# Kernel tuning notes

Measured on AMD Instinct MI355X. Metric: run time of the kernel, lower is better.

Reference implementation:

```python
import jax, jax.numpy as jnp
import numpy as np

NUM_HEADS = 4
D_MODEL = 256
HEAD_DIM = D_MODEL // NUM_HEADS  # 64
B, N = 8, 2048


def _proj(x, W, b):
    # Conv1d with kernel_size=1 == pointwise linear over channel dim
    # x: [B, C_in, N], W: [C_out, C_in], b: [C_out]
    return jnp.einsum('oi,bin->bon', W, x) + b[None, :, None]


def setup_inputs() -> dict:
    key = jax.random.key(0)
    ks = jax.random.split(key, 11)
    s = 1.0 / np.sqrt(D_MODEL)
    return {
        'query': jax.random.normal(ks[0], (B, D_MODEL, N), jnp.float32),
        'key':   jax.random.normal(ks[1], (B, D_MODEL, N), jnp.float32),
        'value': jax.random.normal(ks[2], (B, D_MODEL, N), jnp.float32),
        'Wq': jax.random.normal(ks[3], (D_MODEL, D_MODEL), jnp.float32) * s,
        'bq': jax.random.normal(ks[4], (D_MODEL,), jnp.float32) * 0.01,
        'Wk': jax.random.normal(ks[5], (D_MODEL, D_MODEL), jnp.float32) * s,
        'bk': jax.random.normal(ks[6], (D_MODEL,), jnp.float32) * 0.01,
        'Wv': jax.random.normal(ks[7], (D_MODEL, D_MODEL), jnp.float32) * s,
        'bv': jax.random.normal(ks[8], (D_MODEL,), jnp.float32) * 0.01,
        'Wm': jax.random.normal(ks[9], (D_MODEL, D_MODEL), jnp.float32) * s,
        'bm': jax.random.normal(ks[10], (D_MODEL,), jnp.float32) * 0.01,
    }


def reference(query, key, value, Wq, bq, Wk, bk, Wv, bv, Wm, bm):
    b = query.shape[0]
    # project then split channels into (head_dim, num_heads): [B, d, h, N]
    q = _proj(query, Wq, bq).reshape(b, HEAD_DIM, NUM_HEADS, -1)
    k = _proj(key,   Wk, bk).reshape(b, HEAD_DIM, NUM_HEADS, -1)
    v = _proj(value, Wv, bv).reshape(b, HEAD_DIM, NUM_HEADS, -1)
    scale = 1.0 / jnp.sqrt(jnp.asarray(HEAD_DIM, q.dtype))
    scores = jnp.einsum('bdhn,bdhm->bhnm', q, k) * scale  # [B,H,N,N]
    prob = jax.nn.softmax(scores, axis=-1)
    x = jnp.einsum('bhnm,bdhm->bdhn', prob, v)  # [B,d,H,N]
    x = x.reshape(b, HEAD_DIM * NUM_HEADS, -1)  # [B, d_model, N]
    return _proj(x, Wm, bm)
```

## Files before the change

### kernel.cpp

```cpp
#include <hip/hip_runtime.h>
#include <math.h>


constexpr int BATCH  = 8;
constexpr int DMODEL = 256;
constexpr int SEQ    = 2048;
constexpr int HDIM   = 64;
constexpr int TN     = 128;
constexpr int TM     = 64;
constexpr int NJT    = SEQ / TM;

typedef _Float16 half4_t __attribute__((ext_vector_type(4)));
typedef _Float16 half8_t __attribute__((ext_vector_type(8)));
typedef float    float4_t __attribute__((ext_vector_type(4)));

static __device__ __forceinline__ void ld16_lds(const void* g, void* l) {
    __builtin_amdgcn_global_load_lds(
        (const __attribute__((address_space(1))) unsigned*)g,
        (__attribute__((address_space(3))) unsigned*)l, 16, 0, 0);
}

__global__ __launch_bounds__(256)
void prep_w(const float* __restrict__ Wq, const float* __restrict__ Wk,
            const float* __restrict__ Wv, const float* __restrict__ Wm,
            _Float16* __restrict__ wf)
{
    const int which = blockIdx.y;
    const float* src = which == 0 ? Wq : which == 1 ? Wk : which == 2 ? Wv : Wm;
    const int i = (blockIdx.x * 256 + threadIdx.x) * 4;
    const float4 v = *(const float4*)&src[i];
    half4_t o; o[0] = v.x; o[1] = v.y; o[2] = v.z; o[3] = v.w;
    *(half4_t*)&wf[(size_t)which * DMODEL * DMODEL + i] = o;
}

__global__ __launch_bounds__(256, 3)
void gemm_qkv(const _Float16* __restrict__ wf, const float* __restrict__ bq,
              const float* __restrict__ bk, const float* __restrict__ bv,
              const float* __restrict__ Xq, const float* __restrict__ Xk,
              const float* __restrict__ Xv, _Float16* __restrict__ qT,
              _Float16* __restrict__ kT, _Float16* __restrict__ vT)
{
    const int n0 = blockIdx.x * 64;
    const int proj = blockIdx.y >> 3, b = blockIdx.y & 7;
    const _Float16* W    = wf + (size_t)proj * DMODEL * DMODEL;
    const float*    bias = proj == 0 ? bq : proj == 1 ? bk : bv;
    const float*    X    = (proj == 0 ? Xq : proj == 1 ? Xk : Xv)
                           + (size_t)b * DMODEL * SEQ;
    const float qs = (proj == 0) ? 0.18033688011112042f : 1.0f;

    __shared__ __align__(16) char lds[50432];
    float*    T  = (float*)lds;
    _Float16* Xs = (_Float16*)(lds + 16640);
    _Float16* Tw = (_Float16*)lds;

    const int tid = threadIdx.x, tn = tid & 15, tc = tid >> 4;

    #pragma unroll
    for (int cc = 0; cc < 4; ++cc) {
        __syncthreads();
        #pragma unroll
        for (int i = 0; i < 4; ++i) {
            const int c = tc + 16 * i;
            const float4 v = *(const float4*)&X[(size_t)(cc * 64 + c) * SEQ + n0 + tn * 4];
            T[c * 65 + tn * 4 + 0] = v.x; T[c * 65 + tn * 4 + 1] = v.y;
            T[c * 65 + tn * 4 + 2] = v.z; T[c * 65 + tn * 4 + 3] = v.w;
        }
        __syncthreads();
        #pragma unroll
        for (int i = 0; i < 4; ++i) {
            const int n = tc + 16 * i;
            half4_t h4;
            #pragma unroll
            for (int j = 0; j < 4; ++j) h4[j] = (_Float16)T[(tn * 4 + j) * 65 + n];
            *(half4_t*)&Xs[n * 264 + cc * 64 + tn * 4] = h4;
        }
    }
    __syncthreads();

    const int w = tid >> 6, lane = tid & 63;
    const int lm = lane & 15, g = lane >> 4, g8 = g * 8;
    const int cw0 = w * 64;

    float4_t acc[4][4];
    #pragma unroll
    for (int mt = 0; mt < 4; ++mt)
        #pragma unroll
        for (int nt = 0; nt < 4; ++nt) acc[mt][nt] = (float4_t){0.f, 0.f, 0.f, 0.f};

    #pragma unroll
    for (int k0 = 0; k0 < DMODEL; k0 += 64) {
        half8_t a[4][2], bb[4][2];
        #pragma unroll
        for (int mt = 0; mt < 4; ++mt)
            #pragma unroll
            for (int kd = 0; kd < 2; ++kd)
                a[mt][kd] = *(const half8_t*)&W[(size_t)(cw0 + mt * 16 + lm) * DMODEL
                                                + k0 + kd * 32 + g8];
        #pragma unroll
        for (int nt = 0; nt < 4; ++nt)
            #pragma unroll
            for (int kd = 0; kd < 2; ++kd)
                bb[nt][kd] = *(const half8_t*)&Xs[(nt * 16 + lm) * 264
                                                  + k0 + kd * 32 + g8];
        #pragma unroll
        for (int kd = 0; kd < 2; ++kd)
            #pragma unroll
            for (int mt = 0; mt < 4; ++mt)
                #pragma unroll
                for (int nt = 0; nt < 4; ++nt)
                    acc[mt][nt] = __builtin_amdgcn_mfma_f32_16x16x32_f16(
                        a[mt][kd], bb[nt][kd], acc[mt][nt], 0, 0, 0);
    }
    __syncthreads();

    #pragma unroll
    for (int mt = 0; mt < 4; ++mt) {
        const float4 b4 = *(const float4*)&bias[cw0 + mt * 16 + g * 4];
        const float bb4[4] = {b4.x, b4.y, b4.z, b4.w};
        #pragma unroll
        for (int nt = 0; nt < 4; ++nt) {
            half4_t pk;
            #pragma unroll
            for (int r = 0; r < 4; ++r)
                pk[r] = (_Float16)((acc[mt][nt][r] + bb4[r]) * qs);
            *(half4_t*)&Tw[((w * 64 + nt * 16 + lm)) * 68 + mt * 16 + g * 4] = pk;
        }
    }

    if (proj < 2) {
        _Float16* dst = (proj == 0 ? qT : kT);
        const int h2 = lane >> 4, lml = lane & 15;
        #pragma unroll
        for (int it = 0; it < 4; ++it) {
            const int nl = it * 16 + lml;
            #pragma unroll
            for (int dc = 0; dc < 2; ++dc) {
                half8_t ch;
                #pragma unroll
                for (int e = 0; e < 8; ++e)
                    ch[e] = Tw[(w * 64 + nl) * 68 + 4 * (dc * 8 + e) + h2];
                const int chunk = (w * 2 + dc) ^ (nl & 7);
                *(half8_t*)&dst[((size_t)(b * 4 + h2) * SEQ + n0 + nl) * HDIM
                                + chunk * 8] = ch;
            }
        }
    } else {
        const int hh = lane & 3, dl = (lane >> 2) & 15;
        const int d = w * 16 + dl;
        const int hswap = ((dl >> 3) & 1) << 2;
        const size_t rowbase =
            (((size_t)(b * 4 + hh) * NJT + (n0 >> 6)) * HDIM + d) * (size_t)TM;
        #pragma unroll
        for (int jc = 0; jc < 8; ++jc) {
            half8_t ch;
            #pragma unroll
            for (int e = 0; e < 8; ++e)
                ch[e] = Tw[(w * 64 + jc * 8 + (e ^ hswap)) * 68 + 4 * dl + hh];
            *(half8_t*)&vT[rowbase + ((jc ^ (dl & 7)) << 3)] = ch;
        }
    }
}

__global__ __launch_bounds__(256, 4)
void attn_f16(const _Float16* __restrict__ qT, const _Float16* __restrict__ kT,
              const _Float16* __restrict__ vT, _Float16* __restrict__ xa,
              _Float16* __restrict__ xb, float* __restrict__ rs)
{
    const int lid = blockIdx.x;
    const int work = (lid & 7) * 128 + (lid >> 3);
    const int bh = work >> 5, b = bh >> 2, h = bh & 3;
    const int jh = (work >> 4) & 1;
    const int ib = work & 15;
    const int tid = threadIdx.x, wid = tid >> 6, lane = tid & 63;
    const int lm = lane & 15, g = lane >> 4;
    const int i0 = ib * TN + wid * 32;

    __shared__ _Float16 Kb[2][TM * HDIM];
    __shared__ _Float16 Vb[2][TM * HDIM];

    half8_t bq[2][2];
    const _Float16* qbase = qT + (size_t)bh * SEQ * HDIM;
    #pragma unroll
    for (int rt = 0; rt < 2; ++rt)
        #pragma unroll
        for (int kd = 0; kd < 2; ++kd) {
            const int row = i0 + rt * 16 + lm;
            bq[rt][kd] = *(const half8_t*)(qbase + (size_t)row * HDIM
                                           + (((kd * 4 + g) ^ (lm & 7)) << 3));
        }

    const char* kt = (const char*)(kT + ((size_t)bh * SEQ + jh * (SEQ / 2)) * HDIM);
    const char* vt = (const char*)(vT + ((size_t)bh * NJT + jh * 16) * TM * HDIM);

    float4_t o[2][4];
    float rsum[2] = {0.f, 0.f};
    #pragma unroll
    for (int rt = 0; rt < 2; ++rt)
        #pragma unroll
        for (int dt = 0; dt < 4; ++dt) o[rt][dt] = (float4_t){0.f, 0.f, 0.f, 0.f};

    #define STAGE(jt, bu)                                                     \
        {                                                                     \
            const char* kg = kt + (size_t)(jt) * 8192;                        \
            const char* vg = vt + (size_t)(jt) * 8192;                        \
            _Pragma("unroll")                                                 \
            for (int p = 0; p < 2; ++p) {                                     \
                const int c = wid + p * 4;                                    \
                ld16_lds(kg + c * 1024 + lane * 16, (char*)&Kb[bu][0] + c * 1024); \
                ld16_lds(vg + c * 1024 + lane * 16, (char*)&Vb[bu][0] + c * 1024); \
            }                                                                 \
        }

    STAGE(0, 0);
    __syncthreads();

    for (int jt = 0; jt < 16; ++jt) {
        const int cur = jt & 1;
        if (jt + 1 < 16) STAGE(jt + 1, cur ^ 1);

        float4_t s[4][2];
        #pragma unroll
        for (int ct = 0; ct < 4; ++ct)
            #pragma unroll
            for (int rt = 0; rt < 2; ++rt) s[ct][rt] = (float4_t){0.f, 0.f, 0.f, 0.f};
        #pragma unroll
        for (int kd = 0; kd < 2; ++kd)
            #pragma unroll
            for (int ct = 0; ct < 4; ++ct) {
                const half8_t fk = *(const half8_t*)
                    &Kb[cur][(ct * 16 + lm) * HDIM + (((kd * 4 + g) ^ (lm & 7)) << 3)];
                #pragma unroll
                for (int rt = 0; rt < 2; ++rt)
                    s[ct][rt] = __builtin_amdgcn_mfma_f32_16x16x32_f16(
                        fk, bq[rt][kd], s[ct][rt], 0, 0, 0);
            }

        half4_t ap[4][2];
        #pragma unroll
        for (int ct = 0; ct < 4; ++ct)
            #pragma unroll
            for (int rt = 0; rt < 2; ++rt)
                #pragma unroll
                for (int r = 0; r < 4; ++r) {
                    const float e = __builtin_amdgcn_exp2f(s[ct][rt][r]);
                    rsum[rt] += e;
                    ap[ct][rt][r] = (_Float16)e;
                }

        #pragma unroll
        for (int ct = 0; ct < 4; ++ct)
            #pragma unroll
            for (int dt = 0; dt < 4; ++dt) {
                const int d = dt * 16 + lm;
                const half4_t fv = *(const half4_t*)
                    &Vb[cur][d * TM + ((((ct * 2 + (g >> 1)) ^ (lm & 7)) << 3)
                                       + (((g & 1) ^ (lm >> 3)) << 2))];
                #pragma unroll
                for (int rt = 0; rt < 2; ++rt)
                    o[rt][dt] = __builtin_amdgcn_mfma_f32_16x16x16f16(
                        ap[ct][rt], fv, o[rt][dt], 0, 0, 0);
            }
        __syncthreads();
    }

    _Float16* xp = jh ? xb : xa;
    #pragma unroll
    for (int rt = 0; rt < 2; ++rt)
        #pragma unroll
        for (int dt = 0; dt < 4; ++dt) {
            const int c = 4 * (dt * 16 + lm) + h;
            #pragma unroll
            for (int r = 0; r < 4; ++r) {
                const int n = i0 + rt * 16 + 4 * g + r;
                xp[((size_t)b * SEQ + n) * DMODEL + c] = (_Float16)o[rt][dt][r];
            }
        }
    #pragma unroll
    for (int rt = 0; rt < 2; ++rt) {
        float v = rsum[rt];
        v += __shfl_xor(v, 16);
        v += __shfl_xor(v, 32);
        if (g == 0)
            rs[((size_t)jh * 32 + bh) * SEQ + i0 + rt * 16 + lm] = v;
    }
    #undef STAGE
}

__global__ __launch_bounds__(256)
void gemm_final(const _Float16* __restrict__ wm, const float* __restrict__ bias,
                const _Float16* __restrict__ xa, const _Float16* __restrict__ xb,
                const float* __restrict__ rs, float* __restrict__ out)
{
    const int n0 = blockIdx.x * 64, m0 = blockIdx.y * 128;
    const int b = blockIdx.z;
    const int tid = threadIdx.x, w = tid >> 6, lane = tid & 63;
    const int lm = lane & 15, g = lane >> 4, g8 = g * 8;
    const int cw0 = m0 + w * 32;

    const _Float16* Xa = xa + ((size_t)b * SEQ + n0) * DMODEL;
    const _Float16* Xb2 = xb + ((size_t)b * SEQ + n0) * DMODEL;

    half8_t pm[4];
    #pragma unroll
    for (int nt = 0; nt < 4; ++nt) {
        const int n = n0 + nt * 16 + lm;
        #pragma unroll
        for (int hh = 0; hh < 4; ++hh) {
            const float l = rs[(size_t)(b * 4 + hh) * SEQ + n]
                          + rs[(size_t)(32 + b * 4 + hh) * SEQ + n];
            const _Float16 iv = (_Float16)(1.0f / l);
            pm[nt][hh] = iv; pm[nt][hh + 4] = iv;
        }
    }

    float4_t acc[2][4];
    #pragma unroll
    for (int mt = 0; mt < 2; ++mt)
        #pragma unroll
        for (int nt = 0; nt < 4; ++nt) acc[mt][nt] = (float4_t){0.f, 0.f, 0.f, 0.f};

    #pragma unroll
    for (int k0 = 0; k0 < DMODEL; k0 += 64) {
        half8_t a[2][2], bb[4][2];
        #pragma unroll
        for (int mt = 0; mt < 2; ++mt)
            #pragma unroll
            for (int kd = 0; kd < 2; ++kd)
                a[mt][kd] = *(const half8_t*)&wm[(size_t)(cw0 + mt * 16 + lm) * DMODEL
                                                 + k0 + kd * 32 + g8];
        #pragma unroll
        for (int nt = 0; nt < 4; ++nt)
            #pragma unroll
            for (int kd = 0; kd < 2; ++kd) {
                const size_t off = (size_t)(nt * 16 + lm) * DMODEL + k0 + kd * 32 + g8;
                const half8_t va = *(const half8_t*)&Xa[off];
                const half8_t vb = *(const half8_t*)&Xb2[off];
                bb[nt][kd] = (va + vb) * pm[nt];
            }
        #pragma unroll
        for (int kd = 0; kd < 2; ++kd)
            #pragma unroll
            for (int mt = 0; mt < 2; ++mt)
                #pragma unroll
                for (int nt = 0; nt < 4; ++nt)
                    acc[mt][nt] = __builtin_amdgcn_mfma_f32_16x16x32_f16(
                        a[mt][kd], bb[nt][kd], acc[mt][nt], 0, 0, 0);
    }

    #pragma unroll
    for (int mt = 0; mt < 2; ++mt)
        #pragma unroll
        for (int r = 0; r < 4; ++r) {
            const int co = cw0 + mt * 16 + g * 4 + r;
            const float bv_ = bias[co];
            #pragma unroll
            for (int nt = 0; nt < 4; ++nt)
                out[((size_t)b * DMODEL + co) * SEQ + n0 + nt * 16 + lm] =
                    acc[mt][nt][r] + bv_;
        }
}

extern "C" void kernel_launch(void* const* d_in, const int* in_sizes, int n_in,
                              void* d_out, int out_size, void* d_ws, size_t ws_size,
                              hipStream_t stream) {
    const float* query = (const float*)d_in[0];
    const float* key_  = (const float*)d_in[1];
    const float* value = (const float*)d_in[2];
    const float* Wq = (const float*)d_in[3];  const float* bq = (const float*)d_in[4];
    const float* Wk = (const float*)d_in[5];  const float* bk = (const float*)d_in[6];
    const float* Wv = (const float*)d_in[7];  const float* bv = (const float*)d_in[8];
    const float* Wm = (const float*)d_in[9];  const float* bm = (const float*)d_in[10];
    float* out = (float*)d_out;

    const size_t bufElems = (size_t)BATCH * DMODEL * SEQ;
    _Float16* qT = (_Float16*)d_ws;
    _Float16* kT = qT + bufElems;
    _Float16* vT = kT + bufElems;
    _Float16* xa = vT + bufElems;
    _Float16* xb = xa + bufElems;
    _Float16* wf = xb + bufElems;
    float*    rsb = (float*)(wf + 4 * DMODEL * DMODEL);

    prep_w<<<dim3(DMODEL * DMODEL / 1024, 4), 256, 0, stream>>>(Wq, Wk, Wv, Wm, wf);
    gemm_qkv<<<dim3(SEQ / 64, 3 * BATCH), 256, 0, stream>>>(
        wf, bq, bk, bv, query, key_, value, qT, kT, vT);
    attn_f16<<<dim3(1024), 256, 0, stream>>>(qT, kT, vT, xa, xb, rsb);
    gemm_final<<<dim3(SEQ / 64, 2, BATCH), 256, 0, stream>>>(
        wf + (size_t)3 * DMODEL * DMODEL, bm, xa, xb, rsb, out);
}
```

Measured before the change: 191.1 us.

## Use K=32 MFMA for PV by permuting key rows to match score layout

Reorders which key rows each lane loads in the QK^T MFMA so that the two score tiles form a contiguous 8-element K slice. This lets P·V use the 16x16x32 f16 MFMA with half8 operands instead of 16x16x16 with half4. The XOR swizzles for Q/K layout in the projection kernel change to match, and the V write no longer needs its half-swap. The aim is fewer MFMA issues and wider LDS reads for V, at the cost of more complex index math.

```diff
diff --git a/kernel.cpp b/kernel.cpp
--- a/kernel.cpp
+++ b/kernel.cpp
@@ -133,13 +133,14 @@
         #pragma unroll
         for (int it = 0; it < 4; ++it) {
             const int nl = it * 16 + lml;
+            const int hs = (nl & 3) | (((nl >> 3) & 1) << 2);
             #pragma unroll
             for (int dc = 0; dc < 2; ++dc) {
                 half8_t ch;
                 #pragma unroll
                 for (int e = 0; e < 8; ++e)
                     ch[e] = Tw[(w * 64 + nl) * 68 + 4 * (dc * 8 + e) + h2];
-                const int chunk = (w * 2 + dc) ^ (nl & 7);
+                const int chunk = (w * 2 + dc) ^ hs;
                 *(half8_t*)&dst[((size_t)(b * 4 + h2) * SEQ + n0 + nl) * HDIM
                                 + chunk * 8] = ch;
             }
@@ -147,7 +148,6 @@
     } else {
         const int hh = lane & 3, dl = (lane >> 2) & 15;
         const int d = w * 16 + dl;
-        const int hswap = ((dl >> 3) & 1) << 2;
         const size_t rowbase =
             (((size_t)(b * 4 + hh) * NJT + (n0 >> 6)) * HDIM + d) * (size_t)TM;
         #pragma unroll
@@ -155,7 +155,7 @@
             half8_t ch;
             #pragma unroll
             for (int e = 0; e < 8; ++e)
-                ch[e] = Tw[(w * 64 + jc * 8 + (e ^ hswap)) * 68 + 4 * dl + hh];
+                ch[e] = Tw[(w * 64 + jc * 8 + e) * 68 + 4 * dl + hh];
             *(half8_t*)&vT[rowbase + ((jc ^ (dl & 7)) << 3)] = ch;
         }
     }
@@ -178,6 +178,10 @@
     __shared__ _Float16 Kb[2][TM * HDIM];
     __shared__ _Float16 Vb[2][TM * HDIM];
 
+    const int hq = (lm & 3) | (((lm >> 3) & 1) << 2);
+    const int hk = (lm & 3) | (((lm >> 2) & 1) << 2);
+    const int rbase = 8 * (lm >> 2) + (lm & 3);
+
     half8_t bq[2][2];
     const _Float16* qbase = qT + (size_t)bh * SEQ * HDIM;
     #pragma unroll
@@ -186,14 +190,14 @@
         for (int kd = 0; kd < 2; ++kd) {
             const int row = i0 + rt * 16 + lm;
             bq[rt][kd] = *(const half8_t*)(qbase + (size_t)row * HDIM
-                                           + (((kd * 4 + g) ^ (lm & 7)) << 3));
+                                           + (((kd * 4 + g) ^ hq) << 3));
         }
 
     const char* kt = (const char*)(kT + ((size_t)bh * SEQ + jh * (SEQ / 2)) * HDIM);
     const char* vt = (const char*)(vT + ((size_t)bh * NJT + jh * 16) * TM * HDIM);
 
     float4_t o[2][4];
-    float rsum[2] = {0.f, 0.f};
+    float rsum[2][2] = {{0.f, 0.f}, {0.f, 0.f}};
     #pragma unroll
     for (int rt = 0; rt < 2; ++rt)
         #pragma unroll
@@ -218,47 +222,58 @@
         const int cur = jt & 1;
         if (jt + 1 < 16) STAGE(jt + 1, cur ^ 1);
 
-        float4_t s[4][2];
-        #pragma unroll
-        for (int ct = 0; ct < 4; ++ct)
-            #pragma unroll
-            for (int rt = 0; rt < 2; ++rt) s[ct][rt] = (float4_t){0.f, 0.f, 0.f, 0.f};
+        float4_t s[2][2][2];
+        #pragma unroll
+        for (int jb = 0; jb < 2; ++jb)
+            #pragma unroll
+            for (int u = 0; u < 2; ++u)
+                #pragma unroll
+                for (int rt = 0; rt < 2; ++rt)
+                    s[jb][u][rt] = (float4_t){0.f, 0.f, 0.f, 0.f};
         #pragma unroll
         for (int kd = 0; kd < 2; ++kd)
             #pragma unroll
-            for (int ct = 0; ct < 4; ++ct) {
-                const half8_t fk = *(const half8_t*)
-                    &Kb[cur][(ct * 16 + lm) * HDIM + (((kd * 4 + g) ^ (lm & 7)) << 3)];
-                #pragma unroll
-                for (int rt = 0; rt < 2; ++rt)
-                    s[ct][rt] = __builtin_amdgcn_mfma_f32_16x16x32_f16(
-                        fk, bq[rt][kd], s[ct][rt], 0, 0, 0);
+            for (int jb = 0; jb < 2; ++jb)
+                #pragma unroll
+                for (int u = 0; u < 2; ++u) {
+                    const int jrow = jb * 32 + rbase + 4 * u;
+                    const half8_t fk = *(const half8_t*)
+                        &Kb[cur][jrow * HDIM + (((kd * 4 + g) ^ hk) << 3)];
+                    #pragma unroll
+                    for (int rt = 0; rt < 2; ++rt)
+                        s[jb][u][rt] = __builtin_amdgcn_mfma_f32_16x16x32_f16(
+                            fk, bq[rt][kd], s[jb][u][rt], 0, 0, 0);
+                }
+
+        half8_t ap[2][2];
+        #pragma unroll
+        for (int jb = 0; jb < 2; ++jb)
+            #pragma unroll
+            for (int rt = 0; rt < 2; ++rt) {
+                half8_t p;
+                #pragma unroll
+                for (int r = 0; r < 4; ++r) {
+                    const float e0 = __builtin_amdgcn_exp2f(s[jb][0][rt][r]);
+                    const float e1 = __builtin_amdgcn_exp2f(s[jb][1][rt][r]);
+                    rsum[jb][rt] += e0;
+                    rsum[jb][rt] += e1;
+                    p[r]     = (_Float16)e0;
+                    p[r + 4] = (_Float16)e1;
+                }
+                ap[jb][rt] = p;
             }
 
-        half4_t ap[4][2];
-        #pragma unroll
-        for (int ct = 0; ct < 4; ++ct)
-            #pragma unroll
-            for (int rt = 0; rt < 2; ++rt)
-                #pragma unroll
-                for (int r = 0; r < 4; ++r) {
-                    const float e = __builtin_amdgcn_exp2f(s[ct][rt][r]);
-                    rsum[rt] += e;
-                    ap[ct][rt][r] = (_Float16)e;
-                }
-
-        #pragma unroll
-        for (int ct = 0; ct < 4; ++ct)
+        #pragma unroll
+        for (int jb = 0; jb < 2; ++jb)
             #pragma unroll
             for (int dt = 0; dt < 4; ++dt) {
                 const int d = dt * 16 + lm;
-                const half4_t fv = *(const half4_t*)
-                    &Vb[cur][d * TM + ((((ct * 2 + (g >> 1)) ^ (lm & 7)) << 3)
-                                       + (((g & 1) ^ (lm >> 3)) << 2))];
+                const half8_t fv = *(const half8_t*)
+                    &Vb[cur][d * TM + (((jb * 4 + g) ^ (lm & 7)) << 3)];
                 #pragma unroll
                 for (int rt = 0; rt < 2; ++rt)
-                    o[rt][dt] = __builtin_amdgcn_mfma_f32_16x16x16f16(
-                        ap[ct][rt], fv, o[rt][dt], 0, 0, 0);
+                    o[rt][dt] = __builtin_amdgcn_mfma_f32_16x16x32_f16(
+                        ap[jb][rt], fv, o[rt][dt], 0, 0, 0);
             }
         __syncthreads();
     }
@@ -277,7 +292,7 @@
         }
     #pragma unroll
     for (int rt = 0; rt < 2; ++rt) {
-        float v = rsum[rt];
+        float v = rsum[0][rt] + rsum[1][rt];
         v += __shfl_xor(v, 16);
         v += __shfl_xor(v, 32);
         if (g == 0)
```

New measurement: 188.1 us. Within noise of the previous version (-1.5%).
